# Kernel optimization log

Measured on AMD Instinct MI355X. Metric: run time of the kernel, lower is better.

## Reference

```python
import jax, jax.numpy as jnp
import numpy as np

V, D, H, L, DF = 32000, 768, 12, 12, 3072
B, S, BS = 2, 1024, 16
MASK_ID = V - 1
HD = D // H
STD = 0.02


def setup_inputs() -> dict:
    key = jax.random.key(0)
    ks = jax.random.split(key, 12)
    ids = jax.random.randint(ks[0], (B, S), 0, V)
    m = jax.random.uniform(ks[1], (B, S)) < 0.15
    input_ids = jnp.where(m, MASK_ID, ids)
    target_ids = jax.random.randint(ks[2], (B, S), 0, V)
    noise_level = jax.random.uniform(ks[3], (B,), minval=0.1, maxval=1.0)
    emb = jax.random.normal(ks[4], (V, D)) * STD
    in_w = jax.random.normal(ks[5], (L, 3 * D, D)) * STD
    in_b = jnp.zeros((L, 3 * D))
    attn_out_w = jax.random.normal(ks[6], (L, D, D)) * STD
    attn_out_b = jnp.zeros((L, D))
    ln1_w = jnp.ones((L, D)); ln1_b = jnp.zeros((L, D))
    ln2_w = jnp.ones((L, D)); ln2_b = jnp.zeros((L, D))
    w1 = jax.random.normal(ks[7], (L, DF, D)) * STD; b1 = jnp.zeros((L, DF))
    w2 = jax.random.normal(ks[8], (L, D, DF)) * STD; b2 = jnp.zeros((L, D))
    proj_w = jax.random.normal(ks[9], (V, D)) * STD; proj_b = jnp.zeros((V,))
    return dict(input_ids=input_ids, target_ids=target_ids, noise_level=noise_level,
                emb=emb, in_w=in_w, in_b=in_b, attn_out_w=attn_out_w, attn_out_b=attn_out_b,
                ln1_w=ln1_w, ln1_b=ln1_b, ln2_w=ln2_w, ln2_b=ln2_b,
                w1=w1, b1=b1, w2=w2, b2=b2, proj_w=proj_w, proj_b=proj_b)


def _ln(x, w, b):
    m = x.mean(-1, keepdims=True)
    v = ((x - m) ** 2).mean(-1, keepdims=True)
    return (x - m) / jnp.sqrt(v + 1e-5) * w + b


def _rotary(x):
    # Vectorized equivalent of the per-scalar torch loop: rotates pairs
    # (0,1),(2,3),... within the first rotary_dim = D//2 channels only.
    rd = D // 2
    freqs = 1.0 / (10000.0 ** (jnp.arange(0, rd, 2, dtype=jnp.float32) / rd))  # [rd//2]
    ang = jnp.arange(S, dtype=jnp.float32)[:, None] * freqs[None, :]           # [S, rd//2]
    cos, sin = jnp.cos(ang), jnp.sin(ang)
    xr = x[..., :rd].reshape(B, S, rd // 2, 2)
    x0, x1 = xr[..., 0], xr[..., 1]
    r0 = x0 * cos - x1 * sin
    r1 = x0 * sin + x1 * cos
    rot = jnp.stack([r0, r1], axis=-1).reshape(B, S, rd)
    return jnp.concatenate([rot, x[..., rd:]], axis=-1)


def _block_causal_mask():
    nb = S // BS
    bm = jnp.tril(jnp.ones((nb, nb), dtype=jnp.float32))
    em = jnp.repeat(jnp.repeat(bm, BS, axis=0), BS, axis=1)  # [S, S]
    return (1.0 - em) * -1e9


def _model(input_ids, target_ids, noise_level, emb, in_w, in_b, attn_out_w, attn_out_b,
           ln1_w, ln1_b, ln2_w, ln2_b, w1, b1, w2, b2, proj_w, proj_b):
    x = emb[input_ids]                 # [B, S, D]
    x = _rotary(x)
    mask = _block_causal_mask()        # [S, S] additive
    scale = 1.0 / jnp.sqrt(jnp.float32(HD))
    for l in range(L):
        h = _ln(x, ln1_w[l], ln1_b[l])
        qkv = h @ in_w[l].T + in_b[l]
        q, k, v = jnp.split(qkv, 3, axis=-1)
        q = q.reshape(B, S, H, HD).transpose(0, 2, 1, 3)
        k = k.reshape(B, S, H, HD).transpose(0, 2, 1, 3)
        v = v.reshape(B, S, H, HD).transpose(0, 2, 1, 3)
        scores = jnp.einsum('bhqd,bhkd->bhqk', q, k) * scale + mask
        a = jax.nn.softmax(scores, axis=-1)
        o = jnp.einsum('bhqk,bhkd->bhqd', a, v).transpose(0, 2, 1, 3).reshape(B, S, D)
        x = x + (o @ attn_out_w[l].T + attn_out_b[l])
        h = _ln(x, ln2_w[l], ln2_b[l])
        x = x + (jax.nn.gelu(h @ w1[l].T + b1[l], approximate=False) @ w2[l].T + b2[l])
    logits = x @ proj_w.T + proj_b     # [B, S, V]
    logp = jax.nn.log_softmax(logits, axis=-1)
    ce = -jnp.take_along_axis(logp, target_ids[..., None], axis=-1)[..., 0]  # [B, S]
    is_masked = (input_ids == MASK_ID).astype(logits.dtype)
    weighted = ce * is_masked / noise_level[:, None]
    loss = weighted.sum() / (is_masked.sum() + 1e-8)
    return loss, logits


def reference(input_ids, target_ids, noise_level, emb, in_w, in_b, attn_out_w, attn_out_b,
              ln1_w, ln1_b, ln2_w, ln2_b, w1, b1, w2, b2, proj_w, proj_b):
    return _model(input_ids, target_ids, noise_level, emb, in_w, in_b, attn_out_w, attn_out_b,
                  ln1_w, ln1_b, ln2_w, ln2_b, w1, b1, w2, b2, proj_w, proj_b)
```

## Files before the change

kernel.cpp:

```cpp
#include <hip/hip_runtime.h>
#include <hip/hip_bf16.h>
#include <math.h>

#define V_SZ 32000
#define D_SZ 768
#define H_SZ 12
#define L_SZ 12
#define DF_SZ 3072
#define B_SZ 2
#define S_SZ 1024
#define BS_SZ 16
#define HD_SZ 64
#define MASK_ID 31999
#define NTOK (B_SZ * S_SZ)

typedef __attribute__((ext_vector_type(8))) short bf16x8;
typedef __attribute__((ext_vector_type(4))) short bf16x4;
typedef __attribute__((ext_vector_type(4))) float f32x4;

union B8 { bf16x8 v; __hip_bfloat162 h[4]; };
union B4 { bf16x4 v; __hip_bfloat162 h[2]; };
union U4 { ushort4 u; __hip_bfloat162 h[2]; };
union U4E { ushort4 u; unsigned short e[4]; };

__device__ inline unsigned short f2bf(float x) {
    __hip_bfloat16 b = __float2bfloat16(x);
    union { __hip_bfloat16 b; unsigned short u; } c; c.b = b;
    return c.u;
}

__global__ __launch_bounds__(256) void conv_fold_kernel(
    const float* __restrict__ Wsrc, const float* __restrict__ lnw,
    const float* __restrict__ lnb, const float* __restrict__ bsrc,
    unsigned short* __restrict__ Wdst, float* __restrict__ bdst,
    int rows_per_layer)
{
    const int gw = (blockIdx.x * 256 + threadIdx.x) >> 6;
    const int lane = threadIdx.x & 63;
    const int l = gw / rows_per_layer;
    const float* src = Wsrc + (size_t)gw * D_SZ;
    const float* wv = lnw + l * D_SZ;
    const float* bv = lnb + l * D_SZ;
    unsigned short* dst = Wdst + (size_t)gw * D_SZ;
    float acc = 0.f;
#pragma unroll
    for (int j = 0; j < 3; ++j) {
        int k = lane * 4 + j * 256;
        float4 s = *(const float4*)(src + k);
        float4 w = *(const float4*)(wv + k);
        float4 bb = *(const float4*)(bv + k);
        acc += bb.x * s.x + bb.y * s.y + bb.z * s.z + bb.w * s.w;
        U4 o;
        o.h[0] = __float22bfloat162_rn(float2{s.x * w.x, s.y * w.y});
        o.h[1] = __float22bfloat162_rn(float2{s.z * w.z, s.w * w.w});
        *(ushort4*)(dst + k) = o.u;
    }
#pragma unroll
    for (int off = 32; off; off >>= 1) acc += __shfl_xor(acc, off);
    if (lane == 0) bdst[gw] = bsrc[gw] + acc;
}

__global__ __launch_bounds__(256) void conv_cast_kernel(
    const float* __restrict__ src, unsigned short* __restrict__ dst, int n8)
{
    int i = blockIdx.x * 256 + threadIdx.x;
    if (i >= n8) return;
    const float* p = src + (size_t)i * 8;
    float4 v0 = *(const float4*)p;
    float4 v1 = *(const float4*)(p + 4);
    B8 r;
    r.h[0] = __float22bfloat162_rn(float2{v0.x, v0.y});
    r.h[1] = __float22bfloat162_rn(float2{v0.z, v0.w});
    r.h[2] = __float22bfloat162_rn(float2{v1.x, v1.y});
    r.h[3] = __float22bfloat162_rn(float2{v1.z, v1.w});
    *(bf16x8*)(dst + (size_t)i * 8) = r.v;
}

__global__ __launch_bounds__(256) void embed_rot_kernel(
    const int* __restrict__ ids, const float* __restrict__ emb,
    float* __restrict__ x)
{
    const int tok = blockIdx.x;
    const int s = tok & (S_SZ - 1);
    const int id = ids[tok];
    const float* e = emb + (size_t)id * D_SZ;
    float* xo = x + (size_t)tok * D_SZ;
    const int t = threadIdx.x;

    if (t < 192) {
        float x0 = e[2 * t], x1 = e[2 * t + 1];
        float freq = powf(10000.f, -((float)(2 * t)) / 384.f);
        float ang = (float)s * freq;
        float sn, cs;
        sincosf(ang, &sn, &cs);
        xo[2 * t]     = x0 * cs - x1 * sn;
        xo[2 * t + 1] = x0 * sn + x1 * cs;
    }
    for (int ch = 384 + t; ch < D_SZ; ch += 256) xo[ch] = e[ch];
}

template<int BM, int BN, int AM, int CM, bool WB16, bool XSWZ, bool CEP>
__global__ __launch_bounds__(256) void mfma_gemm(
    const void* __restrict__ Av, const void* __restrict__ Wv,
    const float* __restrict__ bias, const float* __restrict__ Res,
    float* __restrict__ C,
    unsigned short* __restrict__ qp, unsigned short* __restrict__ kp,
    unsigned short* __restrict__ vp, float2* __restrict__ pm,
    int M, int N, int K)
{
    constexpr int MR = BM / 32;
    constexpr int NR = BN / 32;
    constexpr int ACH = BM * 4 / 256;
    constexpr int BCH = BN * 4 / 256;

    __shared__ __align__(16) unsigned short As[2][BM * 32];
    __shared__ __align__(16) unsigned short Bs[2][BN * 32];
    __shared__ float smean[AM == 1 ? BM : 1];
    __shared__ float srstd[AM == 1 ? BM : 1];

    const int tid = threadIdx.x;
    const int lane = tid & 63;
    const int wave = tid >> 6;
    const int wrow0 = (wave >> 1) * (BM / 2);
    const int wcol0 = (wave & 1) * (BN / 2);
    const int kgrp = lane >> 4;
    const int rc = lane & 15;
    const int dsw = ((kgrp - (rc >> 1)) & 3) * 8;

    int m0, n0;
    if constexpr (XSWZ) {
        int id = blockIdx.y * gridDim.x + blockIdx.x;
        int cpx = (gridDim.x * gridDim.y) >> 3;
        int swz = (id & 7) * cpx + (id >> 3);
        m0 = (swz % gridDim.x) * BM;
        n0 = (swz / gridDim.x) * BN;
    } else {
        m0 = blockIdx.x * BM;
        n0 = blockIdx.y * BN;
    }

    if constexpr (AM == 1) {
        const float* A = (const float*)Av;
        const int row = tid >> 2, q = tid & 3;
        const float* xr = A + (size_t)(m0 + row) * K + q * (K >> 2);
        float sum = 0.f, ss = 0.f;
        for (int j = 0; j < (K >> 4); ++j) {
            float4 v = *(const float4*)(xr + j * 4);
            sum += v.x + v.y + v.z + v.w;
            ss += v.x * v.x + v.y * v.y + v.z * v.z + v.w * v.w;
        }
        sum += __shfl_xor(sum, 1); sum += __shfl_xor(sum, 2);
        ss  += __shfl_xor(ss, 1);  ss  += __shfl_xor(ss, 2);
        float mean = sum * (1.f / (float)K);
        float var = ss * (1.f / (float)K) - mean * mean;
        if (q == 0) { smean[row] = mean; srstd[row] = rsqrtf(var + 1e-5f); }
        __syncthreads();
    }

    f32x4 acc[MR][NR];
#pragma unroll
    for (int i = 0; i < MR; ++i)
#pragma unroll
        for (int j = 0; j < NR; ++j) acc[i][j] = (f32x4){0.f, 0.f, 0.f, 0.f};

    float areg[(AM != 2) ? ACH : 1][8];
    bf16x8 areg16[(AM == 2) ? ACH : 1];
    float bregf[WB16 ? 1 : BCH][8];
    bf16x8 breg16[WB16 ? BCH : 1];

    auto load_a = [&](int k0) {
#pragma unroll
        for (int i = 0; i < ACH; ++i) {
            int c = tid + i * 256;
            int row = c >> 2, ksg = ((c & 3) + (c >> 3)) & 3;
            if constexpr (AM == 2) {
                const unsigned short* A16 = (const unsigned short*)Av;
                areg16[i] = *(const bf16x8*)(A16 + (size_t)(m0 + row) * K + k0 + ksg * 8);
            } else {
                const float* p = (const float*)Av + (size_t)(m0 + row) * K + k0 + ksg * 8;
                float4 v0 = *(const float4*)p;
                float4 v1 = *(const float4*)(p + 4);
                areg[i][0] = v0.x; areg[i][1] = v0.y; areg[i][2] = v0.z; areg[i][3] = v0.w;
                areg[i][4] = v1.x; areg[i][5] = v1.y; areg[i][6] = v1.z; areg[i][7] = v1.w;
            }
        }
    };
    auto write_a = [&](int buf) {
#pragma unroll
        for (int i = 0; i < ACH; ++i) {
            int c = tid + i * 256;
            if constexpr (AM == 2) {
                *(bf16x8*)&As[buf][c * 8] = areg16[i];
            } else {
                int row = c >> 2;
                float sc = 1.f, sh = 0.f;
                if constexpr (AM == 1) { sc = srstd[row]; sh = -smean[row] * sc; }
                B8 r;
                r.h[0] = __float22bfloat162_rn(float2{fmaf(areg[i][0], sc, sh), fmaf(areg[i][1], sc, sh)});
                r.h[1] = __float22bfloat162_rn(float2{fmaf(areg[i][2], sc, sh), fmaf(areg[i][3], sc, sh)});
                r.h[2] = __float22bfloat162_rn(float2{fmaf(areg[i][4], sc, sh), fmaf(areg[i][5], sc, sh)});
                r.h[3] = __float22bfloat162_rn(float2{fmaf(areg[i][6], sc, sh), fmaf(areg[i][7], sc, sh)});
                *(bf16x8*)&As[buf][c * 8] = r.v;
            }
        }
    };

    auto load_b = [&](int k0) {
#pragma unroll
        for (int i = 0; i < BCH; ++i) {
            int c = tid + i * 256;
            int row = c >> 2, ksg = ((c & 3) + (c >> 3)) & 3;
            if constexpr (WB16) {
                const unsigned short* W16 = (const unsigned short*)Wv;
                breg16[i] = *(const bf16x8*)(W16 + (size_t)(n0 + row) * K + k0 + ksg * 8);
            } else {
                const float* p = (const float*)Wv + (size_t)(n0 + row) * K + k0 + ksg * 8;
                float4 v0 = *(const float4*)p;
                float4 v1 = *(const float4*)(p + 4);
                bregf[i][0] = v0.x; bregf[i][1] = v0.y; bregf[i][2] = v0.z; bregf[i][3] = v0.w;
                bregf[i][4] = v1.x; bregf[i][5] = v1.y; bregf[i][6] = v1.z; bregf[i][7] = v1.w;
            }
        }
    };
    auto write_b = [&](int buf) {
#pragma unroll
        for (int i = 0; i < BCH; ++i) {
            int c = tid + i * 256;
            if constexpr (WB16) {
                *(bf16x8*)&Bs[buf][c * 8] = breg16[i];
            } else {
                B8 r;
                r.h[0] = __float22bfloat162_rn(float2{bregf[i][0], bregf[i][1]});
                r.h[1] = __float22bfloat162_rn(float2{bregf[i][2], bregf[i][3]});
                r.h[2] = __float22bfloat162_rn(float2{bregf[i][4], bregf[i][5]});
                r.h[3] = __float22bfloat162_rn(float2{bregf[i][6], bregf[i][7]});
                *(bf16x8*)&Bs[buf][c * 8] = r.v;
            }
        }
    };

    auto compute = [&](int buf) {
        bf16x8 af[MR], bf[NR];
#pragma unroll
        for (int mi = 0; mi < MR; ++mi)
            af[mi] = *(const bf16x8*)&As[buf][(wrow0 + mi * 16 + rc) * 32 + dsw];
#pragma unroll
        for (int ni = 0; ni < NR; ++ni)
            bf[ni] = *(const bf16x8*)&Bs[buf][(wcol0 + ni * 16 + rc) * 32 + dsw];
#pragma unroll
        for (int mi = 0; mi < MR; ++mi)
#pragma unroll
            for (int ni = 0; ni < NR; ++ni)
                acc[mi][ni] = __builtin_amdgcn_mfma_f32_16x16x32_bf16(
                    af[mi], bf[ni], acc[mi][ni], 0, 0, 0);
    };

    load_a(0);
    load_b(0);
    write_a(0);
    write_b(0);
    __syncthreads();

    const int nk = K >> 5;
    int cur = 0;
    for (int s = 0; s < nk; ++s) {
        const bool more = (s + 1 < nk);
        const int k1 = (s + 1) << 5;
        if (more) { load_a(k1); load_b(k1); }
        compute(cur);
        if (more) { write_a(cur ^ 1); write_b(cur ^ 1); }
        __syncthreads();
        cur ^= 1;
    }

#pragma unroll
    for (int mi = 0; mi < MR; ++mi) {
#pragma unroll
        for (int ni = 0; ni < NR; ++ni) {
            const int col = n0 + wcol0 + ni * 16 + rc;
            const int rbase = m0 + wrow0 + mi * 16 + kgrp * 4;
            float bv = bias ? bias[col] : 0.f;
            if constexpr (CM == 1) {
                const int region = col / 768;
                const int c768 = col - region * 768;
                const int hh = c768 >> 6, d = c768 & 63;
                const int bb = rbase >> 10, s0 = rbase & 1023;
                const int bh = bb * H_SZ + hh;
                if (region == 0) {
#pragma unroll
                    for (int i = 0; i < 4; ++i)
                        qp[((size_t)(bh << 10) + s0 + i) * 64 + d]
                            = f2bf((acc[mi][ni][i] + bv) * 0.125f);
                } else if (region == 1) {
#pragma unroll
                    for (int i = 0; i < 4; ++i)
                        kp[((size_t)(bh << 10) + s0 + i) * 64 + d]
                            = f2bf(acc[mi][ni][i] + bv);
                } else {
                    U4E t4;
#pragma unroll
                    for (int i = 0; i < 4; ++i) t4.e[i] = f2bf(acc[mi][ni][i] + bv);
                    *(ushort4*)&vp[(((size_t)bh * 64 + d) << 10) + s0] = t4.u;
                }
            } else if constexpr (CM == 2) {
                unsigned short* C16 = (unsigned short*)C;
#pragma unroll
                for (int i = 0; i < 4; ++i) {
                    float v = acc[mi][ni][i] + bv;
                    v = 0.5f * v * (1.f + erff(v * 0.70710678118654752f));
                    C16[(size_t)(rbase + i) * N + col] = f2bf(v);
                }
            } else {
                size_t basei = (size_t)rbase * N + col;
#pragma unroll
                for (int i = 0; i < 4; ++i) {
                    float v = acc[mi][ni][i] + bv;
                    size_t idx = basei + (size_t)i * N;
                    if (Res) v += Res[idx];
                    C[idx] = v;
                }
            }
        }
    }

    if constexpr (CEP) {
        float2 (*sce)[2] = (float2 (*)[2])As;
        float bvv[NR];
#pragma unroll
        for (int ni = 0; ni < NR; ++ni) bvv[ni] = bias[n0 + wcol0 + ni * 16 + rc];
#pragma unroll
        for (int mi = 0; mi < MR; ++mi) {
#pragma unroll
            for (int i = 0; i < 4; ++i) {
                float vmax = -1e30f;
#pragma unroll
                for (int ni = 0; ni < NR; ++ni)
                    vmax = fmaxf(vmax, acc[mi][ni][i] + bvv[ni]);
                vmax = fmaxf(vmax, __shfl_xor(vmax, 1));
                vmax = fmaxf(vmax, __shfl_xor(vmax, 2));
                vmax = fmaxf(vmax, __shfl_xor(vmax, 4));
                vmax = fmaxf(vmax, __shfl_xor(vmax, 8));
                float ssum = 0.f;
#pragma unroll
                for (int ni = 0; ni < NR; ++ni)
                    ssum += __expf(acc[mi][ni][i] + bvv[ni] - vmax);
                ssum += __shfl_xor(ssum, 1);
                ssum += __shfl_xor(ssum, 2);
                ssum += __shfl_xor(ssum, 4);
                ssum += __shfl_xor(ssum, 8);
                if (rc == 0)
                    sce[wrow0 + mi * 16 + kgrp * 4 + i][wave & 1] = float2{vmax, ssum};
            }
        }
        __syncthreads();
        if (tid < BM) {
            float2 a = sce[tid][0], b2 = sce[tid][1];
            float Mv = fmaxf(a.x, b2.x);
            float Sv = a.y * __expf(a.x - Mv) + b2.y * __expf(b2.x - Mv);
            pm[(size_t)(n0 >> 7) * NTOK + m0 + tid] = float2{Mv, Sv};
        }
    }
}

__global__ __launch_bounds__(256) void attn3_kernel(
    const unsigned short* __restrict__ Q16, const unsigned short* __restrict__ K16,
    const unsigned short* __restrict__ VT16, unsigned short* __restrict__ ao16)
{
    const int bid = blockIdx.x;
    const int qb = 63 - bid / 24;
    const int bh = bid % 24;
    const int b = bh / H_SZ, h = bh % H_SZ;
    const int tid = threadIdx.x;
    const int w = tid >> 6, lane = tid & 63;
    const int g = lane >> 4, r = lane & 15;

    constexpr int KS = 72;
    __shared__ __align__(16) unsigned short Pl[4][16 * KS];
    __shared__ float so[4][16][66];
    __shared__ float2 sml[4][16];

    const unsigned short* Qb = Q16 + ((size_t)bh << 10) * 64;
    const unsigned short* Kb = K16 + ((size_t)bh << 10) * 64;
    const unsigned short* Vb = VT16 + ((size_t)bh << 6) * 1024;

    bf16x8 qf[2];
    qf[0] = *(const bf16x8*)&Qb[(qb * 16 + r) * 64 + 8 * g];
    qf[1] = *(const bf16x8*)&Qb[(qb * 16 + r) * 64 + 32 + 8 * g];

    float m_r = -1e30f, l_r = 0.f;
    f32x4 o[4];
#pragma unroll
    for (int ni = 0; ni < 4; ++ni) o[ni] = (f32x4){0.f, 0.f, 0.f, 0.f};

    const int nch = (qb >> 2) + 1;
    const int qbm = qb & 3;

    for (int c = w; c < nch; c += 4) {
        const bool lastc = (c == nch - 1);
        const int mi_hi = lastc ? qbm : 3;

        f32x4 s[4];
#pragma unroll
        for (int mi = 0; mi < 4; ++mi) s[mi] = (f32x4){0.f, 0.f, 0.f, 0.f};
#pragma unroll
        for (int mi = 0; mi < 4; ++mi) {
            if (mi <= mi_hi) {
#pragma unroll
                for (int ks = 0; ks < 2; ++ks) {
                    bf16x8 af = *(const bf16x8*)&Kb[(c * 64 + 16 * mi + r) * 64 + 32 * ks + 8 * g];
                    s[mi] = __builtin_amdgcn_mfma_f32_16x16x32_bf16(af, qf[ks], s[mi], 0, 0, 0);
                }
            }
        }

        float mx = -1e30f;
#pragma unroll
        for (int mi = 0; mi < 4; ++mi) {
            if (mi <= mi_hi) {
#pragma unroll
                for (int i = 0; i < 4; ++i) mx = fmaxf(mx, s[mi][i]);
            }
        }
        mx = fmaxf(mx, __shfl_xor(mx, 16));
        mx = fmaxf(mx, __shfl_xor(mx, 32));
        float m_new = fmaxf(m_r, mx);
        float corr = __expf(m_r - m_new);

        float p[4][4];
        float psum = 0.f;
#pragma unroll
        for (int mi = 0; mi < 4; ++mi) {
#pragma unroll
            for (int i = 0; i < 4; ++i) {
                float pv = (mi <= mi_hi) ? __expf(s[mi][i] - m_new) : 0.f;
                p[mi][i] = pv;
                psum += pv;
            }
        }
        psum += __shfl_xor(psum, 16);
        psum += __shfl_xor(psum, 32);
        l_r = l_r * corr + psum;
        m_r = m_new;

#pragma unroll
        for (int mi = 0; mi < 4; ++mi) {
            B4 t;
            t.h[0] = __float22bfloat162_rn(float2{p[mi][0], p[mi][1]});
            t.h[1] = __float22bfloat162_rn(float2{p[mi][2], p[mi][3]});
            *(bf16x4*)&Pl[w][r * KS + 16 * mi + 4 * g] = t.v;
        }

        float co[4];
#pragma unroll
        for (int i = 0; i < 4; ++i) co[i] = __shfl(corr, 4 * g + i);
#pragma unroll
        for (int ni = 0; ni < 4; ++ni)
#pragma unroll
            for (int i = 0; i < 4; ++i) o[ni][i] *= co[i];

#pragma unroll
        for (int ks = 0; ks < 2; ++ks) {
            if (!lastc || 2 * ks <= qbm) {
                bf16x8 pf = *(const bf16x8*)&Pl[w][r * KS + 32 * ks + 8 * g];
#pragma unroll
                for (int ni = 0; ni < 4; ++ni) {
                    bf16x8 vf = *(const bf16x8*)&Vb[(size_t)(r + 16 * ni) * 1024 + c * 64 + 32 * ks + 8 * g];
                    o[ni] = __builtin_amdgcn_mfma_f32_16x16x32_bf16(pf, vf, o[ni], 0, 0, 0);
                }
            }
        }
    }

    if (g == 0) sml[w][r] = float2{m_r, l_r};
#pragma unroll
    for (int ni = 0; ni < 4; ++ni)
#pragma unroll
        for (int i = 0; i < 4; ++i)
            so[w][4 * g + i][r + 16 * ni] = o[ni][i];
    __syncthreads();

#pragma unroll
    for (int j = 0; j < 4; ++j) {
        int e = tid + j * 256;
        int row = e >> 6, col = e & 63;
        float2 p0 = sml[0][row], p1 = sml[1][row], p2 = sml[2][row], p3 = sml[3][row];
        float M = fmaxf(fmaxf(p0.x, p1.x), fmaxf(p2.x, p3.x));
        float w0 = __expf(p0.x - M), w1 = __expf(p1.x - M);
        float w2 = __expf(p2.x - M), w3 = __expf(p3.x - M);
        float L = p0.y * w0 + p1.y * w1 + p2.y * w2 + p3.y * w3;
        float ov = so[0][row][col] * w0 + so[1][row][col] * w1
                 + so[2][row][col] * w2 + so[3][row][col] * w3;
        ao16[(size_t)(b * S_SZ + qb * 16 + row) * D_SZ + h * HD_SZ + col]
            = f2bf(ov / L);
    }
}

__global__ __launch_bounds__(256) void ce2_kernel(
    const float* __restrict__ logits, const int* __restrict__ tgt,
    const int* __restrict__ inp, const float* __restrict__ noise,
    float* __restrict__ ce_row, float* __restrict__ msk_row)
{
    const int row = blockIdx.x;
    const int t = threadIdx.x;
    const float* lr = logits + (size_t)row * V_SZ;
    const float4* lr4 = (const float4*)lr;

    float m = -1e30f, s = 0.f;
    for (int i = t; i < V_SZ / 4; i += 256) {
        float4 v = lr4[i];
        float mx4 = fmaxf(fmaxf(v.x, v.y), fmaxf(v.z, v.w));
        if (mx4 > m) { s *= __expf(m - mx4); m = mx4; }
        s += __expf(v.x - m) + __expf(v.y - m) + __expf(v.z - m) + __expf(v.w - m);
    }

    __shared__ float sm[256], ss[256];
    sm[t] = m; ss[t] = s;
    __syncthreads();
    for (int off = 128; off; off >>= 1) {
        if (t < off) {
            float m2 = fmaxf(sm[t], sm[t + off]);
            ss[t] = ss[t] * __expf(sm[t] - m2) + ss[t + off] * __expf(sm[t + off] - m2);
            sm[t] = m2;
        }
        __syncthreads();
    }
    if (t == 0) {
        float M = sm[0], S = ss[0];
        int tg = tgt[row];
        float ce = -(lr[tg] - M - logf(S));
        int ism = (inp[row] == MASK_ID) ? 1 : 0;
        int b = row / S_SZ;
        ce_row[row] = ism ? (ce / noise[b]) : 0.f;
        msk_row[row] = ism ? 1.f : 0.f;
    }
}

__global__ __launch_bounds__(64) void ce3_kernel(
    const float2* __restrict__ pm, const float* __restrict__ logits,
    const int* __restrict__ tgt, const int* __restrict__ inp,
    const float* __restrict__ noise, float* __restrict__ ce_row,
    float* __restrict__ msk_row)
{
    const int row = blockIdx.x * 64 + threadIdx.x;
    float m = -1e30f, s = 0.f;
    for (int bb = 0; bb < V_SZ / 128; ++bb) {
        float2 p = pm[(size_t)bb * NTOK + row];
        float M2 = fmaxf(m, p.x);
        s = s * __expf(m - M2) + p.y * __expf(p.x - M2);
        m = M2;
    }
    int tg = tgt[row];
    float lv = logits[(size_t)row * V_SZ + tg];
    float ce = -(lv - m - logf(s));
    int ism = (inp[row] == MASK_ID) ? 1 : 0;
    int b = row / S_SZ;
    ce_row[row] = ism ? (ce / noise[b]) : 0.f;
    msk_row[row] = ism ? 1.f : 0.f;
}

__global__ __launch_bounds__(256) void loss_reduce_kernel(
    const float* __restrict__ ce_row, const float* __restrict__ msk_row,
    float* __restrict__ out0)
{
    const int t = threadIdx.x;
    __shared__ float r1[256], r2[256];
    float s = 0.f, c = 0.f;
    for (int i = t; i < NTOK; i += 256) { s += ce_row[i]; c += msk_row[i]; }
    r1[t] = s; r2[t] = c;
    __syncthreads();
    for (int off = 128; off; off >>= 1) {
        if (t < off) { r1[t] += r1[t + off]; r2[t] += r2[t + off]; }
        __syncthreads();
    }
    if (t == 0) out0[0] = r1[0] / (r2[0] + 1e-8f);
}

extern "C" void kernel_launch(void* const* d_in, const int* in_sizes, int n_in,
                              void* d_out, int out_size, void* d_ws, size_t ws_size,
                              hipStream_t stream)
{
    const int*   input_ids  = (const int*)d_in[0];
    const int*   target_ids = (const int*)d_in[1];
    const float* noise      = (const float*)d_in[2];
    const float* emb        = (const float*)d_in[3];
    const float* in_w       = (const float*)d_in[4];
    const float* in_b       = (const float*)d_in[5];
    const float* aow        = (const float*)d_in[6];
    const float* aob        = (const float*)d_in[7];
    const float* ln1w       = (const float*)d_in[8];
    const float* ln1b       = (const float*)d_in[9];
    const float* ln2w       = (const float*)d_in[10];
    const float* ln2b       = (const float*)d_in[11];
    const float* w1         = (const float*)d_in[12];
    const float* b1         = (const float*)d_in[13];
    const float* w2         = (const float*)d_in[14];
    const float* b2         = (const float*)d_in[15];
    const float* projw      = (const float*)d_in[16];
    const float* projb      = (const float*)d_in[17];

    float* out    = (float*)d_out;
    float* logits = out + 1;

    float* base = out + 4;
    unsigned short* wq16 = (unsigned short*)(base);
    unsigned short* wa16 = (unsigned short*)(base + 10616832);
    unsigned short* w116 = (unsigned short*)(base + 14155776);
    unsigned short* w216 = (unsigned short*)(base + 28311552);
    float* qkvb2 = base + 42467328;
    float* b1b2  = qkvb2 + 27648;
    unsigned short* Q16  = (unsigned short*)(base + 42531840);
    unsigned short* K16  = (unsigned short*)(base + 43318272);
    unsigned short* VT16 = (unsigned short*)(base + 44104704);
    unsigned short* ao16 = (unsigned short*)(base + 44891136);
    unsigned short* mid16= (unsigned short*)(base + 45677568);

    float* x       = (float*)d_ws;
    float* ce_row  = x + (size_t)NTOK * D_SZ;
    float* msk_row = ce_row + NTOK;
    unsigned short* xb16 = (unsigned short*)(msk_row + NTOK);
    unsigned short* projw16 = xb16 + (size_t)NTOK * D_SZ;
    float2* pm = (float2*)d_ws;
    const bool fA = ws_size >= 9453568ull;
    const bool fB = ws_size >= 58605568ull;

    conv_fold_kernel<<<6912, 256, 0, stream>>>(in_w, ln1w, ln1b, in_b, wq16, qkvb2, 2304);
    conv_fold_kernel<<<9216, 256, 0, stream>>>(w1, ln2w, ln2b, b1, w116, b1b2, 3072);
    conv_cast_kernel<<<3456, 256, 0, stream>>>(aow, wa16, 884736);
    conv_cast_kernel<<<13824, 256, 0, stream>>>(w2, w216, 3538944);
    if (fB)
        conv_cast_kernel<<<12000, 256, 0, stream>>>(projw, projw16, 3072000);

    embed_rot_kernel<<<NTOK, 256, 0, stream>>>(input_ids, emb, x);

    for (int l = 0; l < L_SZ; ++l) {
        mfma_gemm<64, 128, 1, 1, true, false, false><<<dim3(32, 18), 256, 0, stream>>>(
            x, wq16 + (size_t)l * 1769472, qkvb2 + l * 2304, nullptr, nullptr,
            Q16, K16, VT16, nullptr, NTOK, 2304, 768);
        attn3_kernel<<<1536, 256, 0, stream>>>(Q16, K16, VT16, ao16);
        mfma_gemm<64, 64, 2, 0, true, false, false><<<dim3(32, 12), 256, 0, stream>>>(
            ao16, wa16 + (size_t)l * 589824, aob + l * D_SZ, x, x,
            nullptr, nullptr, nullptr, nullptr, NTOK, 768, 768);
        mfma_gemm<64, 128, 1, 2, true, false, false><<<dim3(32, 24), 256, 0, stream>>>(
            x, w116 + (size_t)l * 2359296, b1b2 + l * 3072, nullptr, (float*)mid16,
            nullptr, nullptr, nullptr, nullptr, NTOK, 3072, 768);
        mfma_gemm<64, 64, 2, 0, true, false, false><<<dim3(32, 12), 256, 0, stream>>>(
            mid16, w216 + (size_t)l * 2359296, b2 + l * D_SZ, x, x,
            nullptr, nullptr, nullptr, nullptr, NTOK, 768, 3072);
    }

    if (fA)
        conv_cast_kernel<<<768, 256, 0, stream>>>(x, xb16, 196608);

    if (fB) {
        mfma_gemm<128, 128, 2, 0, true, true, true><<<dim3(16, 250), 256, 0, stream>>>(
            xb16, projw16, projb, nullptr, logits,
            nullptr, nullptr, nullptr, pm, NTOK, V_SZ, 768);
        ce3_kernel<<<32, 64, 0, stream>>>(pm, logits, target_ids, input_ids,
                                          noise, ce_row, msk_row);
    } else if (fA) {
        mfma_gemm<128, 128, 2, 0, false, true, true><<<dim3(16, 250), 256, 0, stream>>>(
            xb16, projw, projb, nullptr, logits,
            nullptr, nullptr, nullptr, pm, NTOK, V_SZ, 768);
        ce3_kernel<<<32, 64, 0, stream>>>(pm, logits, target_ids, input_ids,
                                          noise, ce_row, msk_row);
    } else {
        mfma_gemm<128, 128, 0, 0, false, true, false><<<dim3(16, 250), 256, 0, stream>>>(
            x, projw, projb, nullptr, logits,
            nullptr, nullptr, nullptr, nullptr, NTOK, V_SZ, 768);
        ce2_kernel<<<NTOK, 256, 0, stream>>>(logits, target_ids, input_ids, noise,
                                             ce_row, msk_row);
    }

    loss_reduce_kernel<<<1, 256, 0, stream>>>(ce_row, msk_row, out);
}
```

Before: 2.630 ms.

## Drop weight pre-conversion, apply LayerNorm affine in GEMM, split-K FFN2

Removes the upfront passes that folded LayerNorm weights into bf16 copies of the QKV/FFN1 weights and cast the attention-out and FFN2 weights to bf16. The GEMMs now read fp32 weights directly and apply the LN scale and shift on the A-tile load. The FFN2 GEMM is split four ways along K, writing fp32 partial results that a new reduce kernel sums together with the bias and residual. This trades a one-time weight conversion (about 340 MB of traffic) for fp32 weight reads inside every GEMM, plus extra partial-result traffic and one more launch per layer. In exchange the FFN2 grid gets more parallelism.

```diff
diff --git a/kernel.cpp b/kernel.cpp
--- a/kernel.cpp
+++ b/kernel.cpp
@@ -20,44 +20,12 @@
 
 union B8 { bf16x8 v; __hip_bfloat162 h[4]; };
 union B4 { bf16x4 v; __hip_bfloat162 h[2]; };
-union U4 { ushort4 u; __hip_bfloat162 h[2]; };
 union U4E { ushort4 u; unsigned short e[4]; };
 
 __device__ inline unsigned short f2bf(float x) {
     __hip_bfloat16 b = __float2bfloat16(x);
     union { __hip_bfloat16 b; unsigned short u; } c; c.b = b;
     return c.u;
-}
-
-__global__ __launch_bounds__(256) void conv_fold_kernel(
-    const float* __restrict__ Wsrc, const float* __restrict__ lnw,
-    const float* __restrict__ lnb, const float* __restrict__ bsrc,
-    unsigned short* __restrict__ Wdst, float* __restrict__ bdst,
-    int rows_per_layer)
-{
-    const int gw = (blockIdx.x * 256 + threadIdx.x) >> 6;
-    const int lane = threadIdx.x & 63;
-    const int l = gw / rows_per_layer;
-    const float* src = Wsrc + (size_t)gw * D_SZ;
-    const float* wv = lnw + l * D_SZ;
-    const float* bv = lnb + l * D_SZ;
-    unsigned short* dst = Wdst + (size_t)gw * D_SZ;
-    float acc = 0.f;
-#pragma unroll
-    for (int j = 0; j < 3; ++j) {
-        int k = lane * 4 + j * 256;
-        float4 s = *(const float4*)(src + k);
-        float4 w = *(const float4*)(wv + k);
-        float4 bb = *(const float4*)(bv + k);
-        acc += bb.x * s.x + bb.y * s.y + bb.z * s.z + bb.w * s.w;
-        U4 o;
-        o.h[0] = __float22bfloat162_rn(float2{s.x * w.x, s.y * w.y});
-        o.h[1] = __float22bfloat162_rn(float2{s.z * w.z, s.w * w.w});
-        *(ushort4*)(dst + k) = o.u;
-    }
-#pragma unroll
-    for (int off = 32; off; off >>= 1) acc += __shfl_xor(acc, off);
-    if (lane == 0) bdst[gw] = bsrc[gw] + acc;
 }
 
 __global__ __launch_bounds__(256) void conv_cast_kernel(
@@ -99,13 +67,14 @@
     for (int ch = 384 + t; ch < D_SZ; ch += 256) xo[ch] = e[ch];
 }
 
-template<int BM, int BN, int AM, int CM, bool WB16, bool XSWZ, bool CEP>
+template<int BM, int BN, int AM, int CM, bool WB16, bool XSWZ, bool CEP, int SPLITK>
 __global__ __launch_bounds__(256) void mfma_gemm(
     const void* __restrict__ Av, const void* __restrict__ Wv,
     const float* __restrict__ bias, const float* __restrict__ Res,
     float* __restrict__ C,
     unsigned short* __restrict__ qp, unsigned short* __restrict__ kp,
     unsigned short* __restrict__ vp, float2* __restrict__ pm,
+    const float* __restrict__ lnw, const float* __restrict__ lnb,
     int M, int N, int K)
 {
     constexpr int MR = BM / 32;
@@ -138,6 +107,8 @@
         m0 = blockIdx.x * BM;
         n0 = blockIdx.y * BN;
     }
+    const int kdiv = K / SPLITK;
+    const int kbase = (SPLITK > 1) ? blockIdx.z * kdiv : 0;
 
     if constexpr (AM == 1) {
         const float* A = (const float*)Av;
@@ -185,21 +156,41 @@
             }
         }
     };
-    auto write_a = [&](int buf) {
+    auto write_a = [&](int buf, int k0) {
 #pragma unroll
         for (int i = 0; i < ACH; ++i) {
             int c = tid + i * 256;
             if constexpr (AM == 2) {
                 *(bf16x8*)&As[buf][c * 8] = areg16[i];
+            } else if constexpr (AM == 1) {
+                int row = c >> 2, ksg = ((c & 3) + (c >> 3)) & 3;
+                float sc = srstd[row], sh = -smean[row] * sc;
+                const float* lw = lnw + k0 + ksg * 8;
+                const float* lb = lnb + k0 + ksg * 8;
+                float4 w0 = *(const float4*)lw;
+                float4 w1 = *(const float4*)(lw + 4);
+                float4 b0 = *(const float4*)lb;
+                float4 b1 = *(const float4*)(lb + 4);
+                B8 r;
+                r.h[0] = __float22bfloat162_rn(float2{
+                    fmaf(fmaf(areg[i][0], sc, sh), w0.x, b0.x),
+                    fmaf(fmaf(areg[i][1], sc, sh), w0.y, b0.y)});
+                r.h[1] = __float22bfloat162_rn(float2{
+                    fmaf(fmaf(areg[i][2], sc, sh), w0.z, b0.z),
+                    fmaf(fmaf(areg[i][3], sc, sh), w0.w, b0.w)});
+                r.h[2] = __float22bfloat162_rn(float2{
+                    fmaf(fmaf(areg[i][4], sc, sh), w1.x, b1.x),
+                    fmaf(fmaf(areg[i][5], sc, sh), w1.y, b1.y)});
+                r.h[3] = __float22bfloat162_rn(float2{
+                    fmaf(fmaf(areg[i][6], sc, sh), w1.z, b1.z),
+                    fmaf(fmaf(areg[i][7], sc, sh), w1.w, b1.w)});
+                *(bf16x8*)&As[buf][c * 8] = r.v;
             } else {
-                int row = c >> 2;
-                float sc = 1.f, sh = 0.f;
-                if constexpr (AM == 1) { sc = srstd[row]; sh = -smean[row] * sc; }
                 B8 r;
-                r.h[0] = __float22bfloat162_rn(float2{fmaf(areg[i][0], sc, sh), fmaf(areg[i][1], sc, sh)});
-                r.h[1] = __float22bfloat162_rn(float2{fmaf(areg[i][2], sc, sh), fmaf(areg[i][3], sc, sh)});
-                r.h[2] = __float22bfloat162_rn(float2{fmaf(areg[i][4], sc, sh), fmaf(areg[i][5], sc, sh)});
-                r.h[3] = __float22bfloat162_rn(float2{fmaf(areg[i][6], sc, sh), fmaf(areg[i][7], sc, sh)});
+                r.h[0] = __float22bfloat162_rn(float2{areg[i][0], areg[i][1]});
+                r.h[1] = __float22bfloat162_rn(float2{areg[i][2], areg[i][3]});
+                r.h[2] = __float22bfloat162_rn(float2{areg[i][4], areg[i][5]});
+                r.h[3] = __float22bfloat162_rn(float2{areg[i][6], areg[i][7]});
                 *(bf16x8*)&As[buf][c * 8] = r.v;
             }
         }
@@ -255,20 +246,20 @@
                     af[mi], bf[ni], acc[mi][ni], 0, 0, 0);
     };
 
-    load_a(0);
-    load_b(0);
-    write_a(0);
+    load_a(kbase);
+    load_b(kbase);
+    write_a(0, kbase);
     write_b(0);
     __syncthreads();
 
-    const int nk = K >> 5;
+    const int nk = kdiv >> 5;
     int cur = 0;
     for (int s = 0; s < nk; ++s) {
         const bool more = (s + 1 < nk);
-        const int k1 = (s + 1) << 5;
+        const int k1 = kbase + ((s + 1) << 5);
         if (more) { load_a(k1); load_b(k1); }
         compute(cur);
-        if (more) { write_a(cur ^ 1); write_b(cur ^ 1); }
+        if (more) { write_a(cur ^ 1, k1); write_b(cur ^ 1); }
         __syncthreads();
         cur ^= 1;
     }
@@ -279,8 +270,8 @@
         for (int ni = 0; ni < NR; ++ni) {
             const int col = n0 + wcol0 + ni * 16 + rc;
             const int rbase = m0 + wrow0 + mi * 16 + kgrp * 4;
-            float bv = bias ? bias[col] : 0.f;
             if constexpr (CM == 1) {
+                float bv = bias[col];
                 const int region = col / 768;
                 const int c768 = col - region * 768;
                 const int hh = c768 >> 6, d = c768 & 63;
@@ -303,6 +294,7 @@
                     *(ushort4*)&vp[(((size_t)bh * 64 + d) << 10) + s0] = t4.u;
                 }
             } else if constexpr (CM == 2) {
+                float bv = bias[col];
                 unsigned short* C16 = (unsigned short*)C;
 #pragma unroll
                 for (int i = 0; i < 4; ++i) {
@@ -310,7 +302,14 @@
                     v = 0.5f * v * (1.f + erff(v * 0.70710678118654752f));
                     C16[(size_t)(rbase + i) * N + col] = f2bf(v);
                 }
+            } else if constexpr (CM == 3) {
+                float* P = C + (size_t)blockIdx.z * ((size_t)M * N);
+                size_t basei = (size_t)rbase * N + col;
+#pragma unroll
+                for (int i = 0; i < 4; ++i)
+                    P[basei + (size_t)i * N] = acc[mi][ni][i];
             } else {
+                float bv = bias ? bias[col] : 0.f;
                 size_t basei = (size_t)rbase * N + col;
 #pragma unroll
                 for (int i = 0; i < 4; ++i) {
@@ -360,6 +359,30 @@
             pm[(size_t)(n0 >> 7) * NTOK + m0 + tid] = float2{Mv, Sv};
         }
     }
+}
+
+__global__ __launch_bounds__(256) void ffn2_reduce_kernel(
+    const float* __restrict__ pp, const float* __restrict__ bias,
+    float* __restrict__ x)
+{
+    const size_t i = (size_t)(blockIdx.x * 256 + threadIdx.x) * 8;
+    const int col = (int)(i % 768);
+    const size_t E = (size_t)NTOK * D_SZ;
+    float4 s0 = *(const float4*)(x + i);
+    float4 s1 = *(const float4*)(x + i + 4);
+    float4 b0 = *(const float4*)(bias + col);
+    float4 b1 = *(const float4*)(bias + col + 4);
+    s0.x += b0.x; s0.y += b0.y; s0.z += b0.z; s0.w += b0.w;
+    s1.x += b1.x; s1.y += b1.y; s1.z += b1.z; s1.w += b1.w;
+#pragma unroll
+    for (int z = 0; z < 4; ++z) {
+        float4 p0 = *(const float4*)(pp + z * E + i);
+        float4 p1 = *(const float4*)(pp + z * E + i + 4);
+        s0.x += p0.x; s0.y += p0.y; s0.z += p0.z; s0.w += p0.w;
+        s1.x += p1.x; s1.y += p1.y; s1.z += p1.z; s1.w += p1.w;
+    }
+    *(float4*)(x + i) = s0;
+    *(float4*)(x + i + 4) = s1;
 }
 
 __global__ __launch_bounds__(256) void attn3_kernel(
@@ -602,17 +625,12 @@
     float* logits = out + 1;
 
     float* base = out + 4;
-    unsigned short* wq16 = (unsigned short*)(base);
-    unsigned short* wa16 = (unsigned short*)(base + 10616832);
-    unsigned short* w116 = (unsigned short*)(base + 14155776);
-    unsigned short* w216 = (unsigned short*)(base + 28311552);
-    float* qkvb2 = base + 42467328;
-    float* b1b2  = qkvb2 + 27648;
-    unsigned short* Q16  = (unsigned short*)(base + 42531840);
-    unsigned short* K16  = (unsigned short*)(base + 43318272);
-    unsigned short* VT16 = (unsigned short*)(base + 44104704);
-    unsigned short* ao16 = (unsigned short*)(base + 44891136);
-    unsigned short* mid16= (unsigned short*)(base + 45677568);
+    unsigned short* Q16  = (unsigned short*)(base);
+    unsigned short* K16  = (unsigned short*)(base + 786432);
+    unsigned short* VT16 = (unsigned short*)(base + 1572864);
+    unsigned short* ao16 = (unsigned short*)(base + 2359296);
+    unsigned short* mid16= (unsigned short*)(base + 3145728);
+    float* pp            = base + 6291456;
 
     float* x       = (float*)d_ws;
     float* ce_row  = x + (size_t)NTOK * D_SZ;
@@ -623,50 +641,47 @@
     const bool fA = ws_size >= 9453568ull;
     const bool fB = ws_size >= 58605568ull;
 
-    conv_fold_kernel<<<6912, 256, 0, stream>>>(in_w, ln1w, ln1b, in_b, wq16, qkvb2, 2304);
-    conv_fold_kernel<<<9216, 256, 0, stream>>>(w1, ln2w, ln2b, b1, w116, b1b2, 3072);
-    conv_cast_kernel<<<3456, 256, 0, stream>>>(aow, wa16, 884736);
-    conv_cast_kernel<<<13824, 256, 0, stream>>>(w2, w216, 3538944);
     if (fB)
         conv_cast_kernel<<<12000, 256, 0, stream>>>(projw, projw16, 3072000);
 
     embed_rot_kernel<<<NTOK, 256, 0, stream>>>(input_ids, emb, x);
 
     for (int l = 0; l < L_SZ; ++l) {
-        mfma_gemm<64, 128, 1, 1, true, false, false><<<dim3(32, 18), 256, 0, stream>>>(
-            x, wq16 + (size_t)l * 1769472, qkvb2 + l * 2304, nullptr, nullptr,
-            Q16, K16, VT16, nullptr, NTOK, 2304, 768);
+        mfma_gemm<64, 128, 1, 1, false, false, false, 1><<<dim3(32, 18), 256, 0, stream>>>(
+            x, in_w + (size_t)l * 2304 * 768, in_b + l * 2304, nullptr, nullptr,
+            Q16, K16, VT16, nullptr, ln1w + l * 768, ln1b + l * 768, NTOK, 2304, 768);
         attn3_kernel<<<1536, 256, 0, stream>>>(Q16, K16, VT16, ao16);
-        mfma_gemm<64, 64, 2, 0, true, false, false><<<dim3(32, 12), 256, 0, stream>>>(
-            ao16, wa16 + (size_t)l * 589824, aob + l * D_SZ, x, x,
-            nullptr, nullptr, nullptr, nullptr, NTOK, 768, 768);
-        mfma_gemm<64, 128, 1, 2, true, false, false><<<dim3(32, 24), 256, 0, stream>>>(
-            x, w116 + (size_t)l * 2359296, b1b2 + l * 3072, nullptr, (float*)mid16,
-            nullptr, nullptr, nullptr, nullptr, NTOK, 3072, 768);
-        mfma_gemm<64, 64, 2, 0, true, false, false><<<dim3(32, 12), 256, 0, stream>>>(
-            mid16, w216 + (size_t)l * 2359296, b2 + l * D_SZ, x, x,
-            nullptr, nullptr, nullptr, nullptr, NTOK, 768, 3072);
+        mfma_gemm<64, 64, 2, 0, false, false, false, 1><<<dim3(32, 12), 256, 0, stream>>>(
+            ao16, aow + (size_t)l * 768 * 768, aob + l * 768, x, x,
+            nullptr, nullptr, nullptr, nullptr, nullptr, nullptr, NTOK, 768, 768);
+        mfma_gemm<64, 128, 1, 2, false, false, false, 1><<<dim3(32, 24), 256, 0, stream>>>(
+            x, w1 + (size_t)l * 3072 * 768, b1 + l * 3072, nullptr, (float*)mid16,
+            nullptr, nullptr, nullptr, nullptr, ln2w + l * 768, ln2b + l * 768, NTOK, 3072, 768);
+        mfma_gemm<64, 64, 2, 3, false, false, false, 4><<<dim3(32, 12, 4), 256, 0, stream>>>(
+            mid16, w2 + (size_t)l * 768 * 3072, nullptr, nullptr, pp,
+            nullptr, nullptr, nullptr, nullptr, nullptr, nullptr, NTOK, 768, 3072);
+        ffn2_reduce_kernel<<<768, 256, 0, stream>>>(pp, b2 + l * 768, x);
     }
 
     if (fA)
         conv_cast_kernel<<<768, 256, 0, stream>>>(x, xb16, 196608);
 
     if (fB) {
-        mfma_gemm<128, 128, 2, 0, true, true, true><<<dim3(16, 250), 256, 0, stream>>>(
+        mfma_gemm<128, 128, 2, 0, true, true, true, 1><<<dim3(16, 250), 256, 0, stream>>>(
             xb16, projw16, projb, nullptr, logits,
-            nullptr, nullptr, nullptr, pm, NTOK, V_SZ, 768);
+            nullptr, nullptr, nullptr, pm, nullptr, nullptr, NTOK, V_SZ, 768);
         ce3_kernel<<<32, 64, 0, stream>>>(pm, logits, target_ids, input_ids,
                                           noise, ce_row, msk_row);
     } else if (fA) {
-        mfma_gemm<128, 128, 2, 0, false, true, true><<<dim3(16, 250), 256, 0, stream>>>(
+        mfma_gemm<128, 128, 2, 0, false, true, true, 1><<<dim3(16, 250), 256, 0, stream>>>(
             xb16, projw, projb, nullptr, logits,
-            nullptr, nullptr, nullptr, pm, NTOK, V_SZ, 768);
+            nullptr, nullptr, nullptr, pm, nullptr, nullptr, NTOK, V_SZ, 768);
         ce3_kernel<<<32, 64, 0, stream>>>(pm, logits, target_ids, input_ids,
                                           noise, ce_row, msk_row);
     } else {
-        mfma_gemm<128, 128, 0, 0, false, true, false><<<dim3(16, 250), 256, 0, stream>>>(
+        mfma_gemm<128, 128, 0, 0, false, true, false, 1><<<dim3(16, 250), 256, 0, stream>>>(
             x, projw, projb, nullptr, logits,
-            nullptr, nullptr, nullptr, nullptr, NTOK, V_SZ, 768);
+            nullptr, nullptr, nullptr, nullptr, nullptr, nullptr, NTOK, V_SZ, 768);
         ce2_kernel<<<NTOK, 256, 0, stream>>>(logits, target_ids, input_ids, noise,
                                              ce_row, msk_row);
     }
```

After: 2.847 ms. +8.3%, slower.

## Split-K the FFN down-projection GEMM and add a bias-residual reduce kernel

Applied to the files above, without the earlier changes.

Adds a SPLITK template parameter to the MFMA GEMM so the FFN2 GEMM (K=3072) runs with two K-halves across blockIdx.z. Each half writes unbiased fp32 partials to a new workspace region. A new reduce kernel then sums both partials with the bias and the residual into x. The aim is to double the block count for this GEMM and fill the CUs better. In exchange it adds an extra launch per layer, extra global traffic for the partial buffers, and it relies on the workspace being large enough for the new buffer.

```diff
diff --git a/kernel.cpp b/kernel.cpp
--- a/kernel.cpp
+++ b/kernel.cpp
@@ -99,7 +99,7 @@
     for (int ch = 384 + t; ch < D_SZ; ch += 256) xo[ch] = e[ch];
 }
 
-template<int BM, int BN, int AM, int CM, bool WB16, bool XSWZ, bool CEP>
+template<int BM, int BN, int AM, int CM, bool WB16, bool XSWZ, bool CEP, int SPLITK>
 __global__ __launch_bounds__(256) void mfma_gemm(
     const void* __restrict__ Av, const void* __restrict__ Wv,
     const float* __restrict__ bias, const float* __restrict__ Res,
@@ -138,6 +138,8 @@
         m0 = blockIdx.x * BM;
         n0 = blockIdx.y * BN;
     }
+    const int kdiv = K / SPLITK;
+    const int kbase = (SPLITK > 1) ? blockIdx.z * kdiv : 0;
 
     if constexpr (AM == 1) {
         const float* A = (const float*)Av;
@@ -255,17 +257,17 @@
                     af[mi], bf[ni], acc[mi][ni], 0, 0, 0);
     };
 
-    load_a(0);
-    load_b(0);
+    load_a(kbase);
+    load_b(kbase);
     write_a(0);
     write_b(0);
     __syncthreads();
 
-    const int nk = K >> 5;
+    const int nk = kdiv >> 5;
     int cur = 0;
     for (int s = 0; s < nk; ++s) {
         const bool more = (s + 1 < nk);
-        const int k1 = (s + 1) << 5;
+        const int k1 = kbase + ((s + 1) << 5);
         if (more) { load_a(k1); load_b(k1); }
         compute(cur);
         if (more) { write_a(cur ^ 1); write_b(cur ^ 1); }
@@ -279,8 +281,8 @@
         for (int ni = 0; ni < NR; ++ni) {
             const int col = n0 + wcol0 + ni * 16 + rc;
             const int rbase = m0 + wrow0 + mi * 16 + kgrp * 4;
-            float bv = bias ? bias[col] : 0.f;
             if constexpr (CM == 1) {
+                float bv = bias[col];
                 const int region = col / 768;
                 const int c768 = col - region * 768;
                 const int hh = c768 >> 6, d = c768 & 63;
@@ -303,6 +305,7 @@
                     *(ushort4*)&vp[(((size_t)bh * 64 + d) << 10) + s0] = t4.u;
                 }
             } else if constexpr (CM == 2) {
+                float bv = bias[col];
                 unsigned short* C16 = (unsigned short*)C;
 #pragma unroll
                 for (int i = 0; i < 4; ++i) {
@@ -310,7 +313,14 @@
                     v = 0.5f * v * (1.f + erff(v * 0.70710678118654752f));
                     C16[(size_t)(rbase + i) * N + col] = f2bf(v);
                 }
+            } else if constexpr (CM == 3) {
+                float* P = C + (size_t)blockIdx.z * ((size_t)M * N);
+                size_t basei = (size_t)rbase * N + col;
+#pragma unroll
+                for (int i = 0; i < 4; ++i)
+                    P[basei + (size_t)i * N] = acc[mi][ni][i];
             } else {
+                float bv = bias ? bias[col] : 0.f;
                 size_t basei = (size_t)rbase * N + col;
 #pragma unroll
                 for (int i = 0; i < 4; ++i) {
@@ -360,6 +370,30 @@
             pm[(size_t)(n0 >> 7) * NTOK + m0 + tid] = float2{Mv, Sv};
         }
     }
+}
+
+__global__ __launch_bounds__(256) void ffn2_reduce_kernel(
+    const float* __restrict__ pp, const float* __restrict__ bias,
+    float* __restrict__ x)
+{
+    const size_t i = (size_t)(blockIdx.x * 256 + threadIdx.x) * 8;
+    const int col = (int)(i % 768);
+    const size_t E = (size_t)NTOK * D_SZ;
+    float4 s0 = *(const float4*)(x + i);
+    float4 s1 = *(const float4*)(x + i + 4);
+    float4 b0 = *(const float4*)(bias + col);
+    float4 b1 = *(const float4*)(bias + col + 4);
+    s0.x += b0.x; s0.y += b0.y; s0.z += b0.z; s0.w += b0.w;
+    s1.x += b1.x; s1.y += b1.y; s1.z += b1.z; s1.w += b1.w;
+#pragma unroll
+    for (int z = 0; z < 2; ++z) {
+        float4 p0 = *(const float4*)(pp + z * E + i);
+        float4 p1 = *(const float4*)(pp + z * E + i + 4);
+        s0.x += p0.x; s0.y += p0.y; s0.z += p0.z; s0.w += p0.w;
+        s1.x += p1.x; s1.y += p1.y; s1.z += p1.z; s1.w += p1.w;
+    }
+    *(float4*)(x + i) = s0;
+    *(float4*)(x + i + 4) = s1;
 }
 
 __global__ __launch_bounds__(256) void attn3_kernel(
@@ -613,6 +647,7 @@
     unsigned short* VT16 = (unsigned short*)(base + 44104704);
     unsigned short* ao16 = (unsigned short*)(base + 44891136);
     unsigned short* mid16= (unsigned short*)(base + 45677568);
+    float* pp            = base + 48823296;
 
     float* x       = (float*)d_ws;
     float* ce_row  = x + (size_t)NTOK * D_SZ;
@@ -633,38 +668,39 @@
     embed_rot_kernel<<<NTOK, 256, 0, stream>>>(input_ids, emb, x);
 
     for (int l = 0; l < L_SZ; ++l) {
-        mfma_gemm<64, 128, 1, 1, true, false, false><<<dim3(32, 18), 256, 0, stream>>>(
+        mfma_gemm<64, 128, 1, 1, true, false, false, 1><<<dim3(32, 18), 256, 0, stream>>>(
             x, wq16 + (size_t)l * 1769472, qkvb2 + l * 2304, nullptr, nullptr,
             Q16, K16, VT16, nullptr, NTOK, 2304, 768);
         attn3_kernel<<<1536, 256, 0, stream>>>(Q16, K16, VT16, ao16);
-        mfma_gemm<64, 64, 2, 0, true, false, false><<<dim3(32, 12), 256, 0, stream>>>(
+        mfma_gemm<64, 64, 2, 0, true, false, false, 1><<<dim3(32, 12), 256, 0, stream>>>(
             ao16, wa16 + (size_t)l * 589824, aob + l * D_SZ, x, x,
             nullptr, nullptr, nullptr, nullptr, NTOK, 768, 768);
-        mfma_gemm<64, 128, 1, 2, true, false, false><<<dim3(32, 24), 256, 0, stream>>>(
+        mfma_gemm<64, 128, 1, 2, true, false, false, 1><<<dim3(32, 24), 256, 0, stream>>>(
             x, w116 + (size_t)l * 2359296, b1b2 + l * 3072, nullptr, (float*)mid16,
             nullptr, nullptr, nullptr, nullptr, NTOK, 3072, 768);
-        mfma_gemm<64, 64, 2, 0, true, false, false><<<dim3(32, 12), 256, 0, stream>>>(
-            mid16, w216 + (size_t)l * 2359296, b2 + l * D_SZ, x, x,
+        mfma_gemm<64, 64, 2, 3, true, false, false, 2><<<dim3(32, 12, 2), 256, 0, stream>>>(
+            mid16, w216 + (size_t)l * 2359296, nullptr, nullptr, pp,
             nullptr, nullptr, nullptr, nullptr, NTOK, 768, 3072);
+        ffn2_reduce_kernel<<<768, 256, 0, stream>>>(pp, b2 + l * D_SZ, x);
     }
 
     if (fA)
         conv_cast_kernel<<<768, 256, 0, stream>>>(x, xb16, 196608);
 
     if (fB) {
-        mfma_gemm<128, 128, 2, 0, true, true, true><<<dim3(16, 250), 256, 0, stream>>>(
+        mfma_gemm<128, 128, 2, 0, true, true, true, 1><<<dim3(16, 250), 256, 0, stream>>>(
             xb16, projw16, projb, nullptr, logits,
             nullptr, nullptr, nullptr, pm, NTOK, V_SZ, 768);
         ce3_kernel<<<32, 64, 0, stream>>>(pm, logits, target_ids, input_ids,
                                           noise, ce_row, msk_row);
     } else if (fA) {
-        mfma_gemm<128, 128, 2, 0, false, true, true><<<dim3(16, 250), 256, 0, stream>>>(
+        mfma_gemm<128, 128, 2, 0, false, true, true, 1><<<dim3(16, 250), 256, 0, stream>>>(
             xb16, projw, projb, nullptr, logits,
             nullptr, nullptr, nullptr, pm, NTOK, V_SZ, 768);
         ce3_kernel<<<32, 64, 0, stream>>>(pm, logits, target_ids, input_ids,
                                           noise, ce_row, msk_row);
     } else {
-        mfma_gemm<128, 128, 0, 0, false, true, false><<<dim3(16, 250), 256, 0, stream>>>(
+        mfma_gemm<128, 128, 0, 0, false, true, false, 1><<<dim3(16, 250), 256, 0, stream>>>(
             x, projw, projb, nullptr, logits,
             nullptr, nullptr, nullptr, nullptr, NTOK, V_SZ, 768);
         ce2_kernel<<<NTOK, 256, 0, stream>>>(logits, target_ids, input_ids, noise,
```

Result: faster. 2.535 ms (-3.6%).
